# Performance work log

Hardware: AMD Instinct MI355X
Metric: run time of the kernel (lower is better)

The kernel has to match this reference:

```python
import jax, jax.numpy as jnp
import numpy as np

N_HEADS = 16
HEAD_SIZE = 64

def setup_inputs() -> dict:
    key = jax.random.key(0)
    k1, k2 = jax.random.split(key)
    B, N, D = 2, 2048, N_HEADS * HEAD_SIZE
    x = jax.random.normal(k1, (B, N, D), dtype=jnp.float32)
    # lecun_normal-ish scale for the QKV kernel
    W_qkv = jax.random.normal(k2, (D, 3 * D), dtype=jnp.float32) * (1.0 / np.sqrt(D))
    return {"x": x, "W_qkv": W_qkv}

def reference(x, W_qkv):
    B, N, D = x.shape
    H, Dh = N_HEADS, HEAD_SIZE
    qkv = x @ W_qkv                                  # [B,N,3D]
    q, k, v = jnp.split(qkv, 3, axis=-1)
    q = q.reshape(B, N, H, Dh)
    k = k.reshape(B, N, H, Dh)
    v = v.reshape(B, N, H, Dh)
    dist = jnp.einsum('bihd,bjhd->bhij', q, k) / jnp.sqrt(jnp.asarray(Dh, dtype=x.dtype))
    mask = jnp.tril(jnp.ones((N, N), dtype=bool))[None, None, :, :]
    dist = jnp.where(mask, dist, -jnp.inf)
    attn = jax.nn.softmax(dist, axis=-1)             # [B,H,N,N]
    out_heads = jnp.einsum('bhij,bjhd->bihd', attn, v)
    return out_heads.reshape(B, N, H * Dh)
```

## Files before the change

kernel.cpp:

```cpp
#include <hip/hip_runtime.h>

typedef __attribute__((ext_vector_type(8))) short bf16x8;
typedef __attribute__((ext_vector_type(4))) float f32x4;

#define DEVI static __device__ __forceinline__

namespace {
constexpr int NSEQ = 2048, NH = 16;
constexpr int D = 1024, D3 = 3072;
}

DEVI unsigned short f2bf(float f) {
  union { float f; unsigned int u; } v; v.f = f;
  unsigned int r = v.u + 0x7FFFu + ((v.u >> 16) & 1u);
  return (unsigned short)(r >> 16);
}

DEVI void gload16(const unsigned short* g, unsigned short* lds) {
  __builtin_amdgcn_global_load_lds(
      (const __attribute__((address_space(1))) unsigned int*)g,
      (__attribute__((address_space(3))) unsigned int*)lds, 16, 0, 0);
}

DEVI f32x4 mfma16(bf16x8 a, bf16x8 b, f32x4 c) {
  return __builtin_amdgcn_mfma_f32_16x16x32_bf16(a, b, c, 0, 0, 0);
}

DEVI float exp2g(float x) {
#if __has_builtin(__builtin_amdgcn_exp2f)
  return __builtin_amdgcn_exp2f(x);
#else
  return exp2f(x);
#endif
}

DEVI unsigned int cvtpk(float a, float b) {
  unsigned int r;
  asm("v_cvt_pk_bf16_f32 %0, %1, %2" : "=v"(r) : "v"(a), "v"(b));
  return r;
}

__global__ __launch_bounds__(256) void cast_x_k(const float* __restrict__ x,
                                                unsigned short* __restrict__ xb) {
  int i = (blockIdx.x * 256 + threadIdx.x) * 4;
  float4 v = *reinterpret_cast<const float4*>(x + i);
  ushort4 o;
  o.x = f2bf(v.x); o.y = f2bf(v.y); o.z = f2bf(v.z); o.w = f2bf(v.w);
  *reinterpret_cast<ushort4*>(xb + i) = o;
}

__global__ __launch_bounds__(256) void transw_k(const float* __restrict__ W,
                                                unsigned short* __restrict__ Wt) {
  __shared__ float t[32][33];
  int c0 = blockIdx.x * 32, k0 = blockIdx.y * 32;
  int tx = threadIdx.x & 31, ty = threadIdx.x >> 5;
#pragma unroll
  for (int r = 0; r < 32; r += 8)
    t[ty + r][tx] = W[(size_t)(k0 + ty + r) * D3 + c0 + tx];
  __syncthreads();
#pragma unroll
  for (int r = 0; r < 32; r += 8)
    Wt[(size_t)(c0 + ty + r) * D + k0 + tx] = f2bf(t[tx][ty + r]);
}

__global__ __launch_bounds__(256) void qkv_gemm_k(const unsigned short* __restrict__ xb,
                                                  const unsigned short* __restrict__ Wt,
                                                  unsigned short* __restrict__ qw,
                                                  unsigned short* __restrict__ kw,
                                                  unsigned short* __restrict__ vtw) {
  __shared__ unsigned short smA[2][128 * 32];
  __shared__ unsigned short smB[2][128 * 32];
  const int tid = threadIdx.x, w = tid >> 6, l = tid & 63;
  const int m0 = blockIdx.x * 128, n0 = blockIdx.y * 128;
  const int wm = w >> 1, wn = w & 1;

  const unsigned short* ga[2]; const unsigned short* gb[2];
  int lofs[2];
#pragma unroll
  for (int i = 0; i < 2; ++i) {
    int idx = tid + i * 256;
    int row = idx >> 2;
    int blk = (idx & 3) ^ ((row >> 1) & 3);
    ga[i] = xb + (size_t)(m0 + row) * D + blk * 8;
    gb[i] = Wt + (size_t)(n0 + row) * D + blk * 8;
    lofs[i] = (w * 64 + i * 256) * 8;
  }

  f32x4 acc[4][4];
#pragma unroll
  for (int a = 0; a < 4; ++a)
#pragma unroll
    for (int b = 0; b < 4; ++b) acc[a][b] = (f32x4){0.f, 0.f, 0.f, 0.f};

#define GSTAGE(B, KT)                              \
  do {                                             \
    _Pragma("unroll")                              \
    for (int i = 0; i < 2; ++i) {                  \
      gload16(ga[i] + (KT) * 32, smA[B] + lofs[i]);\
      gload16(gb[i] + (KT) * 32, smB[B] + lofs[i]);\
    }                                              \
  } while (0)

  GSTAGE(0, 0);
  for (int kt = 0; kt < D / 32; ++kt) {
    __syncthreads();
    const int cur = kt & 1;
    if (kt + 1 < D / 32) GSTAGE(cur ^ 1, kt + 1);

    bf16x8 af[4], bfr[4];
#pragma unroll
    for (int a = 0; a < 4; ++a) {
      int arow = wm * 64 + a * 16 + (l & 15);
      int blk = (l >> 4) ^ ((arow >> 1) & 3);
      af[a] = *reinterpret_cast<const bf16x8*>(smA[cur] + arow * 32 + blk * 8);
    }
#pragma unroll
    for (int b = 0; b < 4; ++b) {
      int brow = wn * 64 + b * 16 + (l & 15);
      int blk = (l >> 4) ^ ((brow >> 1) & 3);
      bfr[b] = *reinterpret_cast<const bf16x8*>(smB[cur] + brow * 32 + blk * 8);
    }
#pragma unroll
    for (int a = 0; a < 4; ++a)
#pragma unroll
      for (int b = 0; b < 4; ++b)
        acc[a][b] = mfma16(af[a], bfr[b], acc[a][b]);
  }
#undef GSTAGE

  const int which = n0 >> 10;
#pragma unroll
  for (int a = 0; a < 4; ++a) {
#pragma unroll
    for (int b = 0; b < 4; ++b) {
#pragma unroll
      for (int r = 0; r < 4; ++r) {
        int grow = m0 + wm * 64 + a * 16 + (l >> 4) * 4 + r;
        int gcol = n0 + wn * 64 + b * 16 + (l & 15);
        float v = acc[a][b][r];
        int bb = grow >> 11, n = grow & 2047;
        int cc = gcol & 1023, h = cc >> 6, dh = cc & 63;
        size_t bh = (size_t)bb * NH + h;
        if (which == 0)
          qw[(bh * NSEQ + n) * 64 + dh] = f2bf(v * 0.18033688011112042f);
        else if (which == 1)
          kw[(bh * NSEQ + n) * 64 + dh] = f2bf(v);
        else
          vtw[(bh * 64 + dh) * NSEQ + n] = f2bf(v);
      }
    }
  }
}

__global__ __launch_bounds__(256, 4) void attn_k(const unsigned short* __restrict__ qw,
                                                 const unsigned short* __restrict__ kw,
                                                 const unsigned short* __restrict__ vtw,
                                                 float* __restrict__ out) {
  __shared__ unsigned short smK[2][64 * 64];
  __shared__ unsigned short smV[2][64 * 64];
  __shared__ unsigned short smP[4][16 * 64];
  const int tid = threadIdx.x, w = tid >> 6, l = tid & 63;
  const int g = l >> 4, ql = l & 15;
  const int qx = (ql & 7) << 4;

  const int wg = blockIdx.x;
  const int xcd = wg & 7, s = wg >> 3;
  const int bhl = s >> 5;
  const int s5 = s & 31;
  const int j = (s5 + 5 * bhl) & 31;
  const int qt = (j & 1) ? (j >> 1) : (31 - (j >> 1));
  const int bh = xcd * 4 + bhl;
  const int b = bh >> 4, h = bh & 15;
  const int qbase = qt * 64;

  const unsigned short* qb = qw + (size_t)bh * NSEQ * 64;
  const unsigned short* kb = kw + (size_t)bh * NSEQ * 64;
  const unsigned short* vb = vtw + (size_t)bh * 64 * NSEQ;
  char* pl = (char*)smP[w];

  const int i0 = tid, i1 = tid + 256;
  const int r0 = i0 >> 3, c0 = (i0 & 7) ^ (r0 & 7);
  const int r1 = i1 >> 3, c1 = (i1 & 7) ^ (r1 & 7);

  const int qrow = qbase + w * 16 + ql;
  const bf16x8 qf0 = *reinterpret_cast<const bf16x8*>(qb + (size_t)qrow * 64 + g * 8);
  const bf16x8 qf1 = *reinterpret_cast<const bf16x8*>(qb + (size_t)qrow * 64 + 32 + g * 8);

  float m = -1e30f, lsum = 0.f;
  f32x4 o[4];
#pragma unroll
  for (int c = 0; c < 4; ++c) o[c] = (f32x4){0.f, 0.f, 0.f, 0.f};

#define STAGE(B, T)                                                               \
  do {                                                                            \
    gload16(kb + ((size_t)(T) * 64 + r0) * 64 + c0 * 8, smK[B] + w * 512);        \
    gload16(vb + (size_t)r0 * NSEQ + (T) * 64 + c0 * 8, smV[B] + w * 512);        \
    gload16(kb + ((size_t)(T) * 64 + r1) * 64 + c1 * 8, smK[B] + w * 512 + 2048); \
    gload16(vb + (size_t)r1 * NSEQ + (T) * 64 + c1 * 8, smV[B] + w * 512 + 2048); \
  } while (0)

  STAGE(0, 0);
  for (int t = 0; t <= qt; ++t) {
    __syncthreads();
    const int cur = t & 1;
    if (t < qt) STAGE(cur ^ 1, t + 1);

    const unsigned short* K = smK[cur];
    const unsigned short* V = smV[cur];

    f32x4 sc4[4];
#pragma unroll
    for (int c = 0; c < 4; ++c) sc4[c] = (f32x4){0.f, 0.f, 0.f, 0.f};
    __builtin_amdgcn_s_setprio(1);
#pragma unroll
    for (int c = 0; c < 4; ++c) {
      const int krow = c * 16 + ql, sw = krow & 7;
      bf16x8 kf0 = *reinterpret_cast<const bf16x8*>(K + krow * 64 + ((g ^ sw) * 8));
      bf16x8 kf1 = *reinterpret_cast<const bf16x8*>(K + krow * 64 + (((4 + g) ^ sw) * 8));
      sc4[c] = mfma16(kf0, qf0, sc4[c]);
      sc4[c] = mfma16(kf1, qf1, sc4[c]);
    }
    __builtin_amdgcn_s_setprio(0);

    if (t == qt) {
      const int qloc = w * 16 + ql;
#pragma unroll
      for (int c = 0; c < 4; ++c)
#pragma unroll
        for (int r = 0; r < 4; ++r)
          if (c * 16 + g * 4 + r > qloc) sc4[c][r] = -1e30f;
    }

    float tmax = sc4[0][0];
#pragma unroll
    for (int c = 0; c < 4; ++c)
#pragma unroll
      for (int r = 0; r < 4; ++r) tmax = fmaxf(tmax, sc4[c][r]);
    tmax = fmaxf(tmax, __shfl_xor(tmax, 16, 64));
    tmax = fmaxf(tmax, __shfl_xor(tmax, 32, 64));

    if (!__all(tmax <= m + 8.0f)) {
      const float mn = fmaxf(m, tmax);
      const float sc = exp2g(m - mn);
      m = mn;
      lsum *= sc;
      float sco[4];
#pragma unroll
      for (int r = 0; r < 4; ++r) sco[r] = __shfl(sc, (l & 48) + g * 4 + r, 64);
#pragma unroll
      for (int c = 0; c < 4; ++c)
#pragma unroll
        for (int r = 0; r < 4; ++r) o[c][r] *= sco[r];
    }

    float rsum = 0.f;
#pragma unroll
    for (int c = 0; c < 4; ++c) {
      float p0 = exp2g(sc4[c][0] - m), p1 = exp2g(sc4[c][1] - m);
      float p2 = exp2g(sc4[c][2] - m), p3 = exp2g(sc4[c][3] - m);
      rsum += (p0 + p1) + (p2 + p3);
      unsigned int u0 = cvtpk(p0, p1), u1 = cvtpk(p2, p3);
      *reinterpret_cast<uint2*>(pl + ql * 128 + ((32 * c + 8 * g) ^ qx)) =
          make_uint2(u0, u1);
    }
    rsum += __shfl_xor(rsum, 16, 64);
    rsum += __shfl_xor(rsum, 32, 64);
    lsum += rsum;

    asm volatile("s_waitcnt lgkmcnt(0)" ::: "memory");
    __builtin_amdgcn_sched_barrier(0);

    bf16x8 pf0 = *reinterpret_cast<const bf16x8*>(pl + ql * 128 + ((16 * g) ^ qx));
    bf16x8 pf1 = *reinterpret_cast<const bf16x8*>(pl + ql * 128 + ((64 + 16 * g) ^ qx));
    __builtin_amdgcn_s_setprio(1);
#pragma unroll
    for (int c = 0; c < 4; ++c) {
      const int vrow = c * 16 + ql, sw = vrow & 7;
      bf16x8 vf0 = *reinterpret_cast<const bf16x8*>(V + vrow * 64 + ((g ^ sw) * 8));
      bf16x8 vf1 = *reinterpret_cast<const bf16x8*>(V + vrow * 64 + (((4 + g) ^ sw) * 8));
      o[c] = mfma16(pf0, vf0, o[c]);
      o[c] = mfma16(pf1, vf1, o[c]);
    }
    __builtin_amdgcn_s_setprio(0);
  }
#undef STAGE

  const float linv = 1.0f / lsum;
  float lo4[4];
#pragma unroll
  for (int r = 0; r < 4; ++r) lo4[r] = __shfl(linv, (l & 48) + g * 4 + r, 64);
#pragma unroll
  for (int c = 0; c < 4; ++c) {
#pragma unroll
    for (int r = 0; r < 4; ++r) {
      const int n = qbase + w * 16 + g * 4 + r;
      const int dh = c * 16 + ql;
      out[((size_t)b * NSEQ + n) * D + h * 64 + dh] = o[c][r] * lo4[r];
    }
  }
}

extern "C" void kernel_launch(void* const* d_in, const int* in_sizes, int n_in,
                              void* d_out, int out_size, void* d_ws, size_t ws_size,
                              hipStream_t stream) {
  const float* x = (const float*)d_in[0];
  const float* W = (const float*)d_in[1];
  float* out = (float*)d_out;
  char* ws = (char*)d_ws;
  unsigned short* xb  = (unsigned short*)(ws);
  unsigned short* Wt  = (unsigned short*)(ws + 8388608);
  unsigned short* qw  = (unsigned short*)(ws + 14680064);
  unsigned short* kw  = (unsigned short*)(ws + 23068672);
  unsigned short* vtw = (unsigned short*)(ws + 31457280);

  cast_x_k<<<4096, 256, 0, stream>>>(x, xb);
  transw_k<<<dim3(96, 32), 256, 0, stream>>>(W, Wt);
  qkv_gemm_k<<<dim3(32, 24), 256, 0, stream>>>(xb, Wt, qw, kw, vtw);
  attn_k<<<1024, 256, 0, stream>>>(qw, kw, vtw, out);
}
```

Measured before the change: 101.5 us.

## Rewrite QKV GEMM as 256x256 tile with phased LDS pipeline; merge prep kernels

The QKV projection GEMM moves from 128x128 tiles with 4 waves and a K-step of 32 to 256x256 tiles with 8 waves and a K-step of 64. It uses a double-buffered, half-split LDS layout with an XOR swizzle and an explicitly scheduled ping-pong of barriers, setprio and waitcnt that interleaves global-to-LDS loads with MFMA phases. The x cast and W transpose kernels are merged into a single launch to cut launch overhead. The larger tiles use more LDS and registers and launch only 192 blocks, which raises the risk of low occupancy and poor CU coverage. The hand-scheduled waitcnt counts are fragile.

```diff
diff --git a/kernel.cpp b/kernel.cpp
--- a/kernel.cpp
+++ b/kernel.cpp
@@ -40,104 +40,160 @@
   return r;
 }
 
-__global__ __launch_bounds__(256) void cast_x_k(const float* __restrict__ x,
-                                                unsigned short* __restrict__ xb) {
-  int i = (blockIdx.x * 256 + threadIdx.x) * 4;
-  float4 v = *reinterpret_cast<const float4*>(x + i);
-  ushort4 o;
-  o.x = f2bf(v.x); o.y = f2bf(v.y); o.z = f2bf(v.z); o.w = f2bf(v.w);
-  *reinterpret_cast<ushort4*>(xb + i) = o;
-}
-
-__global__ __launch_bounds__(256) void transw_k(const float* __restrict__ W,
-                                                unsigned short* __restrict__ Wt) {
+__global__ __launch_bounds__(256) void prep_k(const float* __restrict__ x,
+                                              const float* __restrict__ W,
+                                              unsigned short* __restrict__ xb,
+                                              unsigned short* __restrict__ Wt) {
   __shared__ float t[32][33];
-  int c0 = blockIdx.x * 32, k0 = blockIdx.y * 32;
-  int tx = threadIdx.x & 31, ty = threadIdx.x >> 5;
-#pragma unroll
-  for (int r = 0; r < 32; r += 8)
-    t[ty + r][tx] = W[(size_t)(k0 + ty + r) * D3 + c0 + tx];
-  __syncthreads();
-#pragma unroll
-  for (int r = 0; r < 32; r += 8)
-    Wt[(size_t)(c0 + ty + r) * D + k0 + tx] = f2bf(t[tx][ty + r]);
-}
-
-__global__ __launch_bounds__(256) void qkv_gemm_k(const unsigned short* __restrict__ xb,
-                                                  const unsigned short* __restrict__ Wt,
-                                                  unsigned short* __restrict__ qw,
-                                                  unsigned short* __restrict__ kw,
-                                                  unsigned short* __restrict__ vtw) {
-  __shared__ unsigned short smA[2][128 * 32];
-  __shared__ unsigned short smB[2][128 * 32];
+  const int bid = blockIdx.x;
+  if (bid < 4096) {
+    int i = (bid * 256 + threadIdx.x) * 4;
+    float4 v = *reinterpret_cast<const float4*>(x + i);
+    ushort4 o;
+    o.x = f2bf(v.x); o.y = f2bf(v.y); o.z = f2bf(v.z); o.w = f2bf(v.w);
+    *reinterpret_cast<ushort4*>(xb + i) = o;
+  } else {
+    const int b2 = bid - 4096;
+    const int c0 = (b2 % 96) * 32, k0 = (b2 / 96) * 32;
+    const int tx = threadIdx.x & 31, ty = threadIdx.x >> 5;
+#pragma unroll
+    for (int r = 0; r < 32; r += 8)
+      t[ty + r][tx] = W[(size_t)(k0 + ty + r) * D3 + c0 + tx];
+    __syncthreads();
+#pragma unroll
+    for (int r = 0; r < 32; r += 8)
+      Wt[(size_t)(c0 + ty + r) * D + k0 + tx] = f2bf(t[tx][ty + r]);
+  }
+}
+
+__global__ __launch_bounds__(512, 2) void qkv_gemm_k(const unsigned short* __restrict__ xb,
+                                                     const unsigned short* __restrict__ Wt,
+                                                     unsigned short* __restrict__ qw,
+                                                     unsigned short* __restrict__ kw,
+                                                     unsigned short* __restrict__ vtw) {
+  __shared__ unsigned short smA[2][2][128 * 64];
+  __shared__ unsigned short smB[2][2][128 * 64];
   const int tid = threadIdx.x, w = tid >> 6, l = tid & 63;
-  const int m0 = blockIdx.x * 128, n0 = blockIdx.y * 128;
-  const int wm = w >> 1, wn = w & 1;
-
-  const unsigned short* ga[2]; const unsigned short* gb[2];
-  int lofs[2];
-#pragma unroll
-  for (int i = 0; i < 2; ++i) {
-    int idx = tid + i * 256;
-    int row = idx >> 2;
-    int blk = (idx & 3) ^ ((row >> 1) & 3);
-    ga[i] = xb + (size_t)(m0 + row) * D + blk * 8;
-    gb[i] = Wt + (size_t)(n0 + row) * D + blk * 8;
-    lofs[i] = (w * 64 + i * 256) * 8;
-  }
-
-  f32x4 acc[4][4];
-#pragma unroll
-  for (int a = 0; a < 4; ++a)
-#pragma unroll
-    for (int b = 0; b < 4; ++b) acc[a][b] = (f32x4){0.f, 0.f, 0.f, 0.f};
-
-#define GSTAGE(B, KT)                              \
-  do {                                             \
-    _Pragma("unroll")                              \
-    for (int i = 0; i < 2; ++i) {                  \
-      gload16(ga[i] + (KT) * 32, smA[B] + lofs[i]);\
-      gload16(gb[i] + (KT) * 32, smB[B] + lofs[i]);\
-    }                                              \
-  } while (0)
-
-  GSTAGE(0, 0);
-  for (int kt = 0; kt < D / 32; ++kt) {
-    __syncthreads();
-    const int cur = kt & 1;
-    if (kt + 1 < D / 32) GSTAGE(cur ^ 1, kt + 1);
-
-    bf16x8 af[4], bfr[4];
-#pragma unroll
-    for (int a = 0; a < 4; ++a) {
-      int arow = wm * 64 + a * 16 + (l & 15);
-      int blk = (l >> 4) ^ ((arow >> 1) & 3);
-      af[a] = *reinterpret_cast<const bf16x8*>(smA[cur] + arow * 32 + blk * 8);
-    }
-#pragma unroll
-    for (int b = 0; b < 4; ++b) {
-      int brow = wn * 64 + b * 16 + (l & 15);
-      int blk = (l >> 4) ^ ((brow >> 1) & 3);
-      bfr[b] = *reinterpret_cast<const bf16x8*>(smB[cur] + brow * 32 + blk * 8);
-    }
-#pragma unroll
-    for (int a = 0; a < 4; ++a)
-#pragma unroll
-      for (int b = 0; b < 4; ++b)
-        acc[a][b] = mfma16(af[a], bfr[b], acc[a][b]);
-  }
-#undef GSTAGE
+  const int wm = w >> 2, wn = w & 3;
+  const int g = l >> 4, ql = l & 15;
+  const int m0 = blockIdx.x * 256, n0 = blockIdx.y * 256;
+
+  const int laneF0 = ql * 64 + ((g ^ (ql & 7)) << 3);
+  const int laneF1 = ql * 64 + (((4 + g) ^ (ql & 7)) << 3);
+
+  const int sr = tid >> 3;
+  const int sc = (tid & 7) ^ (sr & 7);
+  const unsigned short* gA = xb + (size_t)(m0 + sr) * D + sc * 8;
+  const unsigned short* gB = Wt + (size_t)(n0 + sr) * D + sc * 8;
+  const int w512 = w * 512;
+
+  f32x4 acc[8][4];
+#pragma unroll
+  for (int i = 0; i < 8; ++i)
+#pragma unroll
+    for (int j = 0; j < 4; ++j) acc[i][j] = (f32x4){0.f, 0.f, 0.f, 0.f};
+
+  bf16x8 af[4][2], bf0[2][2], bf1[2][2];
+
+#define RDA(db, mh)                                                            \
+  do {                                                                         \
+    _Pragma("unroll") for (int i_ = 0; i_ < 4; ++i_) {                         \
+      af[i_][0] = *(const bf16x8*)&smA[db][wm][((mh)*4 + i_) * 1024 + laneF0]; \
+      af[i_][1] = *(const bf16x8*)&smA[db][wm][((mh)*4 + i_) * 1024 + laneF1]; \
+    }                                                                          \
+  } while (0)
+#define RDB(db, nh, BF)                                                        \
+  do {                                                                         \
+    _Pragma("unroll") for (int i_ = 0; i_ < 2; ++i_) {                         \
+      BF[i_][0] = *(const bf16x8*)&smB[db][wn >> 1][(wn & 1) * 4096 +          \
+                                                    ((nh)*2 + i_) * 1024 + laneF0]; \
+      BF[i_][1] = *(const bf16x8*)&smB[db][wn >> 1][(wn & 1) * 4096 +          \
+                                                    ((nh)*2 + i_) * 1024 + laneF1]; \
+    }                                                                          \
+  } while (0)
+#define QUAD(mh, nh, BF)                                                       \
+  do {                                                                         \
+    _Pragma("unroll") for (int i_ = 0; i_ < 4; ++i_)                           \
+    _Pragma("unroll") for (int j_ = 0; j_ < 2; ++j_) {                         \
+      acc[(mh)*4 + i_][(nh)*2 + j_] =                                          \
+          mfma16(af[i_][0], BF[j_][0], acc[(mh)*4 + i_][(nh)*2 + j_]);         \
+      acc[(mh)*4 + i_][(nh)*2 + j_] =                                          \
+          mfma16(af[i_][1], BF[j_][1], acc[(mh)*4 + i_][(nh)*2 + j_]);         \
+    }                                                                          \
+  } while (0)
+#define STG_A(db, half, t)                                                     \
+  do {                                                                         \
+    gload16(gA + (half)*131072 + (t)*64, &smA[db][half][w512]);                \
+    gload16(gA + (half)*131072 + 65536 + (t)*64, &smA[db][half][w512 + 4096]); \
+  } while (0)
+#define STG_B(db, half, t)                                                     \
+  do {                                                                         \
+    gload16(gB + (half)*131072 + (t)*64, &smB[db][half][w512]);                \
+    gload16(gB + (half)*131072 + 65536 + (t)*64, &smB[db][half][w512 + 4096]); \
+  } while (0)
+#define PH_OPEN                                                                \
+  __builtin_amdgcn_s_barrier();                                                \
+  asm volatile("s_waitcnt lgkmcnt(0)" ::: "memory");                           \
+  __builtin_amdgcn_sched_barrier(0);                                           \
+  __builtin_amdgcn_s_setprio(1)
+#define PH_CLOSE                                                               \
+  __builtin_amdgcn_s_setprio(0);                                               \
+  __builtin_amdgcn_sched_barrier(0);                                           \
+  __builtin_amdgcn_s_barrier();                                                \
+  __builtin_amdgcn_sched_barrier(0)
+#define PH_CLOSE_VM                                                            \
+  __builtin_amdgcn_s_setprio(0);                                               \
+  asm volatile("s_waitcnt vmcnt(2)" ::: "memory");                             \
+  __builtin_amdgcn_sched_barrier(0);                                           \
+  __builtin_amdgcn_s_barrier();                                                \
+  __builtin_amdgcn_sched_barrier(0)
+
+  STG_A(0, 0, 0); STG_A(0, 1, 0); STG_B(0, 0, 0); STG_B(0, 1, 0);
+  STG_A(1, 0, 1);
+  asm volatile("s_waitcnt vmcnt(2)" ::: "memory");
+  __builtin_amdgcn_s_barrier();
+  __builtin_amdgcn_sched_barrier(0);
+
+  for (int it = 0; it < 8; ++it) {
+    const int tO = 2 * it + 1;
+    const int tE2 = (2 * it + 2) & 15;
+    const int tO2 = (2 * it + 3) & 15;
+    RDA(0, 0); RDB(0, 0, bf0); STG_A(1, 1, tO);
+    PH_OPEN; QUAD(0, 0, bf0); PH_CLOSE;
+    RDB(0, 1, bf1); STG_B(1, 0, tO);
+    PH_OPEN; QUAD(0, 1, bf1); PH_CLOSE;
+    RDA(0, 1); STG_B(1, 1, tO);
+    PH_OPEN; QUAD(1, 1, bf1); PH_CLOSE;
+    RDB(0, 0, bf0); STG_A(0, 0, tE2);
+    PH_OPEN; QUAD(1, 0, bf0); PH_CLOSE_VM;
+    RDA(1, 0); RDB(1, 0, bf0); STG_A(0, 1, tE2);
+    PH_OPEN; QUAD(0, 0, bf0); PH_CLOSE;
+    RDB(1, 1, bf1); STG_B(0, 0, tE2);
+    PH_OPEN; QUAD(0, 1, bf1); PH_CLOSE;
+    RDA(1, 1); STG_B(0, 1, tE2);
+    PH_OPEN; QUAD(1, 1, bf1); PH_CLOSE;
+    RDB(1, 0, bf0); STG_A(1, 0, tO2);
+    PH_OPEN; QUAD(1, 0, bf0); PH_CLOSE_VM;
+  }
+#undef RDA
+#undef RDB
+#undef QUAD
+#undef STG_A
+#undef STG_B
+#undef PH_OPEN
+#undef PH_CLOSE
+#undef PH_CLOSE_VM
 
   const int which = n0 >> 10;
 #pragma unroll
-  for (int a = 0; a < 4; ++a) {
-#pragma unroll
-    for (int b = 0; b < 4; ++b) {
+  for (int mf = 0; mf < 8; ++mf) {
+#pragma unroll
+    for (int nf = 0; nf < 4; ++nf) {
 #pragma unroll
       for (int r = 0; r < 4; ++r) {
-        int grow = m0 + wm * 64 + a * 16 + (l >> 4) * 4 + r;
-        int gcol = n0 + wn * 64 + b * 16 + (l & 15);
-        float v = acc[a][b][r];
+        int grow = m0 + wm * 128 + mf * 16 + g * 4 + r;
+        int gcol = n0 + wn * 64 + nf * 16 + ql;
+        float v = acc[mf][nf][r];
         int bb = grow >> 11, n = grow & 2047;
         int cc = gcol & 1023, h = cc >> 6, dh = cc & 63;
         size_t bh = (size_t)bb * NH + h;
@@ -313,8 +369,7 @@
   unsigned short* kw  = (unsigned short*)(ws + 23068672);
   unsigned short* vtw = (unsigned short*)(ws + 31457280);
 
-  cast_x_k<<<4096, 256, 0, stream>>>(x, xb);
-  transw_k<<<dim3(96, 32), 256, 0, stream>>>(W, Wt);
-  qkv_gemm_k<<<dim3(32, 24), 256, 0, stream>>>(xb, Wt, qw, kw, vtw);
+  prep_k<<<7168, 256, 0, stream>>>(x, W, xb, Wt);
+  qkv_gemm_k<<<dim3(16, 12), 512, 0, stream>>>(xb, Wt, qw, kw, vtw);
   attn_k<<<1024, 256, 0, stream>>>(qw, kw, vtw, out);
 }
```

Measured after the change: 115.6 us. 13.8% more time.

## Merge cast and transpose kernels; single-buffer QKV GEMM LDS staging

Applied to the files above, without the earlier changes.

Combines the x-cast and W-transpose kernels into one launch that dispatches on block index, removing one kernel launch and its boundary. The QKV GEMM drops its double-buffered LDS prefetch in favour of a single buffer: each k-step loads the tile, waits on vmcnt(0), syncs, then computes. This halves LDS use, which could raise occupancy, but global loads no longer overlap MFMA work.

```diff
diff --git a/kernel.cpp b/kernel.cpp
--- a/kernel.cpp
+++ b/kernel.cpp
@@ -40,27 +40,30 @@
   return r;
 }
 
-__global__ __launch_bounds__(256) void cast_x_k(const float* __restrict__ x,
-                                                unsigned short* __restrict__ xb) {
-  int i = (blockIdx.x * 256 + threadIdx.x) * 4;
-  float4 v = *reinterpret_cast<const float4*>(x + i);
-  ushort4 o;
-  o.x = f2bf(v.x); o.y = f2bf(v.y); o.z = f2bf(v.z); o.w = f2bf(v.w);
-  *reinterpret_cast<ushort4*>(xb + i) = o;
-}
-
-__global__ __launch_bounds__(256) void transw_k(const float* __restrict__ W,
-                                                unsigned short* __restrict__ Wt) {
+__global__ __launch_bounds__(256) void prep_k(const float* __restrict__ x,
+                                              const float* __restrict__ W,
+                                              unsigned short* __restrict__ xb,
+                                              unsigned short* __restrict__ Wt) {
   __shared__ float t[32][33];
-  int c0 = blockIdx.x * 32, k0 = blockIdx.y * 32;
-  int tx = threadIdx.x & 31, ty = threadIdx.x >> 5;
-#pragma unroll
-  for (int r = 0; r < 32; r += 8)
-    t[ty + r][tx] = W[(size_t)(k0 + ty + r) * D3 + c0 + tx];
-  __syncthreads();
-#pragma unroll
-  for (int r = 0; r < 32; r += 8)
-    Wt[(size_t)(c0 + ty + r) * D + k0 + tx] = f2bf(t[tx][ty + r]);
+  const int bid = blockIdx.x;
+  if (bid < 4096) {
+    int i = (bid * 256 + threadIdx.x) * 4;
+    float4 v = *reinterpret_cast<const float4*>(x + i);
+    ushort4 o;
+    o.x = f2bf(v.x); o.y = f2bf(v.y); o.z = f2bf(v.z); o.w = f2bf(v.w);
+    *reinterpret_cast<ushort4*>(xb + i) = o;
+  } else {
+    const int b2 = bid - 4096;
+    const int c0 = (b2 % 96) * 32, k0 = (b2 / 96) * 32;
+    const int tx = threadIdx.x & 31, ty = threadIdx.x >> 5;
+#pragma unroll
+    for (int r = 0; r < 32; r += 8)
+      t[ty + r][tx] = W[(size_t)(k0 + ty + r) * D3 + c0 + tx];
+    __syncthreads();
+#pragma unroll
+    for (int r = 0; r < 32; r += 8)
+      Wt[(size_t)(c0 + ty + r) * D + k0 + tx] = f2bf(t[tx][ty + r]);
+  }
 }
 
 __global__ __launch_bounds__(256) void qkv_gemm_k(const unsigned short* __restrict__ xb,
@@ -68,14 +71,14 @@
                                                   unsigned short* __restrict__ qw,
                                                   unsigned short* __restrict__ kw,
                                                   unsigned short* __restrict__ vtw) {
-  __shared__ unsigned short smA[2][128 * 32];
-  __shared__ unsigned short smB[2][128 * 32];
+  __shared__ unsigned short smA[128 * 32];
+  __shared__ unsigned short smB[128 * 32];
   const int tid = threadIdx.x, w = tid >> 6, l = tid & 63;
   const int m0 = blockIdx.x * 128, n0 = blockIdx.y * 128;
   const int wm = w >> 1, wn = w & 1;
 
   const unsigned short* ga[2]; const unsigned short* gb[2];
-  int lofs[2];
+  unsigned short* la[2]; unsigned short* lb[2];
 #pragma unroll
   for (int i = 0; i < 2; ++i) {
     int idx = tid + i * 256;
@@ -83,7 +86,8 @@
     int blk = (idx & 3) ^ ((row >> 1) & 3);
     ga[i] = xb + (size_t)(m0 + row) * D + blk * 8;
     gb[i] = Wt + (size_t)(n0 + row) * D + blk * 8;
-    lofs[i] = (w * 64 + i * 256) * 8;
+    la[i] = smA + (w * 64 + i * 256) * 8;
+    lb[i] = smB + (w * 64 + i * 256) * 8;
   }
 
   f32x4 acc[4][4];
@@ -92,33 +96,28 @@
 #pragma unroll
     for (int b = 0; b < 4; ++b) acc[a][b] = (f32x4){0.f, 0.f, 0.f, 0.f};
 
-#define GSTAGE(B, KT)                              \
-  do {                                             \
-    _Pragma("unroll")                              \
-    for (int i = 0; i < 2; ++i) {                  \
-      gload16(ga[i] + (KT) * 32, smA[B] + lofs[i]);\
-      gload16(gb[i] + (KT) * 32, smB[B] + lofs[i]);\
-    }                                              \
-  } while (0)
-
-  GSTAGE(0, 0);
   for (int kt = 0; kt < D / 32; ++kt) {
     __syncthreads();
-    const int cur = kt & 1;
-    if (kt + 1 < D / 32) GSTAGE(cur ^ 1, kt + 1);
+#pragma unroll
+    for (int i = 0; i < 2; ++i) {
+      gload16(ga[i] + kt * 32, la[i]);
+      gload16(gb[i] + kt * 32, lb[i]);
+    }
+    asm volatile("s_waitcnt vmcnt(0)" ::: "memory");
+    __syncthreads();
 
     bf16x8 af[4], bfr[4];
 #pragma unroll
     for (int a = 0; a < 4; ++a) {
       int arow = wm * 64 + a * 16 + (l & 15);
       int blk = (l >> 4) ^ ((arow >> 1) & 3);
-      af[a] = *reinterpret_cast<const bf16x8*>(smA[cur] + arow * 32 + blk * 8);
+      af[a] = *reinterpret_cast<const bf16x8*>(smA + arow * 32 + blk * 8);
     }
 #pragma unroll
     for (int b = 0; b < 4; ++b) {
       int brow = wn * 64 + b * 16 + (l & 15);
       int blk = (l >> 4) ^ ((brow >> 1) & 3);
-      bfr[b] = *reinterpret_cast<const bf16x8*>(smB[cur] + brow * 32 + blk * 8);
+      bfr[b] = *reinterpret_cast<const bf16x8*>(smB + brow * 32 + blk * 8);
     }
 #pragma unroll
     for (int a = 0; a < 4; ++a)
@@ -126,7 +125,6 @@
       for (int b = 0; b < 4; ++b)
         acc[a][b] = mfma16(af[a], bfr[b], acc[a][b]);
   }
-#undef GSTAGE
 
   const int which = n0 >> 10;
 #pragma unroll
@@ -313,8 +311,7 @@
   unsigned short* kw  = (unsigned short*)(ws + 23068672);
   unsigned short* vtw = (unsigned short*)(ws + 31457280);
 
-  cast_x_k<<<4096, 256, 0, stream>>>(x, xb);
-  transw_k<<<dim3(96, 32), 256, 0, stream>>>(W, Wt);
+  prep_k<<<7168, 256, 0, stream>>>(x, W, xb, Wt);
   qkv_gemm_k<<<dim3(32, 24), 256, 0, stream>>>(xb, Wt, qw, kw, vtw);
   attn_k<<<1024, 256, 0, stream>>>(qw, kw, vtw, out);
 }
```

Result: faster. 91.96 us (-9.4%).
